# Optimization experiments

Measured on AMD Instinct MI355X. Metric: run time of the kernel, lower is better.

## Reference

```python
import jax, jax.numpy as jnp
import numpy as np

B, S, H, D = 2, 2048, 16, 64
HID = H * D
NEG = -1e9


def _rope(q, cos, sin):
    # q: (B,S,H,D); cos/sin: (S, D//2) -> broadcast (1,S,1,D//2)
    qe, qo = q[..., 0::2], q[..., 1::2]
    c = cos[None, :, None, :]
    s = sin[None, :, None, :]
    oe = qe * c - qo * s
    oo = qe * s + qo * c
    return jnp.stack([oe, oo], axis=-1).reshape(q.shape)  # interleave even/odd pairs


def setup_inputs() -> dict:
    key = jax.random.key(0)
    ks = jax.random.split(key, 9)
    scale = 1.0 / np.sqrt(HID)
    x = jax.random.normal(ks[0], (B, S, HID), jnp.float32)
    Wq = jax.random.normal(ks[1], (HID, HID), jnp.float32) * scale
    Wk = jax.random.normal(ks[2], (HID, HID), jnp.float32) * scale
    Wv = jax.random.normal(ks[3], (HID, HID), jnp.float32) * scale
    Wo = jax.random.normal(ks[4], (HID, HID), jnp.float32) * scale
    bq = jnp.zeros((HID,), jnp.float32)
    bk = jnp.zeros((HID,), jnp.float32)
    bv = jnp.zeros((HID,), jnp.float32)
    bo = jnp.zeros((HID,), jnp.float32)
    # standard RoPE angles: theta_i = 10000^{-2i/D}
    inv_freq = 1.0 / (10000.0 ** (np.arange(0, D, 2, dtype=np.float32) / D))  # (D/2,)
    angles = jnp.arange(S, dtype=jnp.float32)[:, None] * jnp.asarray(inv_freq)[None, :]
    freqs_cos = jnp.cos(angles)
    freqs_sin = jnp.sin(angles)
    causal = jnp.tril(jnp.ones((S, S), bool))
    mask = jnp.where(causal, 0.0, NEG).astype(jnp.float32)[None, None]  # (1,1,S,S)
    return dict(x=x, Wq=Wq, bq=bq, Wk=Wk, bk=bk, Wv=Wv, bv=bv, Wo=Wo, bo=bo,
                mask=mask, freqs_cos=freqs_cos, freqs_sin=freqs_sin)


def reference(x, Wq, bq, Wk, bk, Wv, bv, Wo, bo, mask, freqs_cos, freqs_sin):
    b, s, hid = x.shape
    # weights stored (in, out): y = x @ W + b (equivalent to torch Linear with W^T)
    q = (x @ Wq + bq).reshape(b, s, H, D)
    k = (x @ Wk + bk).reshape(b, s, H, D)
    v = (x @ Wv + bv).reshape(b, s, H, D)
    q = _rope(q, freqs_cos, freqs_sin)
    k = _rope(k, freqs_cos, freqs_sin)
    q = q.transpose(0, 2, 1, 3)  # (B,H,S,D)
    k = k.transpose(0, 2, 1, 3)
    v = v.transpose(0, 2, 1, 3)
    scores = jnp.einsum('bhqd,bhkd->bhqk', q, k) / np.sqrt(D)
    scores = scores + mask
    attn = jax.nn.softmax(scores.astype(jnp.float32), axis=-1)
    out = jnp.einsum('bhqk,bhkd->bhqd', attn, v)
    out = out.transpose(0, 2, 1, 3).reshape(b, s, hid)
    return out @ Wo + bo
```

## Files before the change

### kernel.cpp

```cpp
#include <hip/hip_runtime.h>
#include <hip/hip_bf16.h>

#define BDIM 2
#define SDIM 2048
#define HDIM 16
#define DDIM 64
#define HID  1024
#define MDIM (BDIM * SDIM)

typedef __attribute__((ext_vector_type(8))) short short8;
typedef __attribute__((ext_vector_type(4))) short short4v;
typedef __attribute__((ext_vector_type(4))) float f32x4;
typedef __attribute__((ext_vector_type(2))) unsigned int uint2v;

__device__ __forceinline__ float bf2f(short u) {
    union { unsigned int i; float f; } x;
    x.i = ((unsigned int)(unsigned short)u) << 16;
    return x.f;
}
__device__ __forceinline__ short f2bf(float f) {
    union { float f; unsigned int i; } x; x.f = f;
    unsigned int r = x.i + 0x7fffu + ((x.i >> 16) & 1u);
    return (short)(r >> 16);
}
__device__ __forceinline__ unsigned int cvtpk_bf16(float lo, float hi) {
    unsigned int r;
    asm("v_cvt_pk_bf16_f32 %0, %1, %2" : "=v"(r) : "v"(lo), "v"(hi));
    return r;
}
__device__ __forceinline__ int swz(int row, int c8) {
    return row * 64 + ((c8 ^ (row & 7)) << 3);
}

__global__ __launch_bounds__(256) void cvt_bf16(const float* __restrict__ in,
                                               short* __restrict__ out, int n) {
    int i = (blockIdx.x * 256 + threadIdx.x) * 8;
    if (i >= n) return;
    float4 a = *(const float4*)(in + i);
    float4 b = *(const float4*)(in + i + 4);
    short8 v;
    v[0] = f2bf(a.x); v[1] = f2bf(a.y); v[2] = f2bf(a.z); v[3] = f2bf(a.w);
    v[4] = f2bf(b.x); v[5] = f2bf(b.y); v[6] = f2bf(b.z); v[7] = f2bf(b.w);
    *(short8*)(out + i) = v;
}

__global__ __launch_bounds__(256) void transpose4(
    const float* __restrict__ w0, const float* __restrict__ w1,
    const float* __restrict__ w2, const float* __restrict__ w3,
    short* __restrict__ o0, short* __restrict__ o1,
    short* __restrict__ o2, short* __restrict__ o3)
{
    const float* src; short* dst;
    int z = blockIdx.z;
    if (z == 0)      { src = w0; dst = o0; }
    else if (z == 1) { src = w1; dst = o1; }
    else if (z == 2) { src = w2; dst = o2; }
    else             { src = w3; dst = o3; }
    __shared__ float t[64][65];
    int r0 = blockIdx.y * 64, c0 = blockIdx.x * 64;
    int rd_r = threadIdx.x >> 4, rd_c = (threadIdx.x & 15) * 4;
    #pragma unroll
    for (int it = 0; it < 4; it++) {
        int rr = rd_r + it * 16;
        float4 v = *(const float4*)(src + (size_t)(r0 + rr) * HID + c0 + rd_c);
        t[rr][rd_c + 0] = v.x; t[rr][rd_c + 1] = v.y;
        t[rr][rd_c + 2] = v.z; t[rr][rd_c + 3] = v.w;
    }
    __syncthreads();
    int or_ = threadIdx.x >> 3, oc8 = (threadIdx.x & 7) * 8;
    #pragma unroll
    for (int half = 0; half < 2; half++) {
        int dr = or_ + half * 32;
        short8 v;
        #pragma unroll
        for (int i = 0; i < 8; i++) v[i] = f2bf(t[oc8 + i][dr]);
        *(short8*)(dst + (size_t)(c0 + dr) * HID + r0 + oc8) = v;
    }
}

__global__ __launch_bounds__(256) void gemm_bf16(
    const short* __restrict__ X,
    const short* __restrict__ Wt0,
    const float* __restrict__ b0, const float* __restrict__ b1, const float* __restrict__ b2,
    const float* __restrict__ cosb, const float* __restrict__ sinb,
    short* __restrict__ out0, float* __restrict__ outf,
    int modeBase)
{
    constexpr int LDK = 40;
    __shared__ __align__(16) short Asm[2][128 * LDK];
    __shared__ __align__(16) short Bsm[2][128 * LDK];
    int z = blockIdx.z;
    int mode = modeBase + z;
    const short* Wt = Wt0 + (size_t)z * HID * HID;
    const float* bias = (z == 0) ? b0 : (z == 1) ? b1 : b2;
    short* outp = out0 + (size_t)z * MDIM * HID;

    int tid = threadIdx.x;
    int lane = tid & 63, wave = tid >> 6;
    int wr = wave >> 1, wc = wave & 1;
    int m0 = blockIdx.x * 128, n0 = blockIdx.y * 128;
    int sr = tid >> 2, sc = (tid & 3) * 8;
    int lr = lane & 15, lg = lane >> 4;

    const short* ax = X  + (size_t)(m0 + sr) * HID + sc;
    const short* bx = Wt + (size_t)(n0 + sr) * HID + sc;
    int wA = sr * LDK + sc, wA2 = (sr + 64) * LDK + sc;

    f32x4 acc[4][4] = {};
    constexpr int NK = HID / 32;

    short8 a0, a1, b0v, b1v;
    a0  = *(const short8*)(ax);
    a1  = *(const short8*)(ax + (size_t)64 * HID);
    b0v = *(const short8*)(bx);
    b1v = *(const short8*)(bx + (size_t)64 * HID);
    *(short8*)(Asm[0] + wA)  = a0;
    *(short8*)(Asm[0] + wA2) = a1;
    *(short8*)(Bsm[0] + wA)  = b0v;
    *(short8*)(Bsm[0] + wA2) = b1v;
    a0  = *(const short8*)(ax + 32);
    a1  = *(const short8*)(ax + (size_t)64 * HID + 32);
    b0v = *(const short8*)(bx + 32);
    b1v = *(const short8*)(bx + (size_t)64 * HID + 32);

    int cur = 0;
    for (int ki = 0; ki < NK; ki++) {
        __syncthreads();
        if (ki + 1 < NK) {
            *(short8*)(Asm[cur ^ 1] + wA)  = a0;
            *(short8*)(Asm[cur ^ 1] + wA2) = a1;
            *(short8*)(Bsm[cur ^ 1] + wA)  = b0v;
            *(short8*)(Bsm[cur ^ 1] + wA2) = b1v;
        }
        if (ki + 2 < NK) {
            int k0 = (ki + 2) * 32;
            a0  = *(const short8*)(ax + k0);
            a1  = *(const short8*)(ax + (size_t)64 * HID + k0);
            b0v = *(const short8*)(bx + k0);
            b1v = *(const short8*)(bx + (size_t)64 * HID + k0);
        }
        short8 af[4], bfr[4];
        #pragma unroll
        for (int m = 0; m < 4; m++)
            af[m] = *(const short8*)(Asm[cur] + (wr * 64 + m * 16 + lr) * LDK + lg * 8);
        #pragma unroll
        for (int n = 0; n < 4; n++)
            bfr[n] = *(const short8*)(Bsm[cur] + (wc * 64 + n * 16 + lr) * LDK + lg * 8);
        __builtin_amdgcn_s_setprio(1);
        #pragma unroll
        for (int m = 0; m < 4; m++)
            #pragma unroll
            for (int n = 0; n < 4; n++)
                acc[m][n] = __builtin_amdgcn_mfma_f32_16x16x32_bf16(af[m], bfr[n], acc[m][n], 0, 0, 0);
        __builtin_amdgcn_s_setprio(0);
        cur ^= 1;
    }

    #pragma unroll
    for (int m = 0; m < 4; m++) {
        #pragma unroll
        for (int n = 0; n < 4; n++) {
            int gr0 = m0 + wr * 64 + m * 16 + lg * 4;
            int gc  = n0 + wc * 64 + n * 16 + lr;
            if (mode == 3) {
                #pragma unroll
                for (int j = 0; j < 4; j++)
                    outf[(size_t)(gr0 + j) * HID + gc] = acc[m][n][j] + bias[gc];
            } else if (mode == 2) {
                int bb = gr0 >> 11, s0 = gr0 & (SDIM - 1);
                int h = gc >> 6, dd = gc & 63;
                short4v pk;
                #pragma unroll
                for (int j = 0; j < 4; j++) pk[j] = f2bf(acc[m][n][j] + bias[gc]);
                *(short4v*)(outp + ((size_t)((bb * HDIM + h) * DDIM + dd)) * SDIM + s0) = pk;
            } else {
                #pragma unroll
                for (int j = 0; j < 4; j++) {
                    int gr = gr0 + j;
                    int bb = gr >> 11, s = gr & (SDIM - 1);
                    int h = gc >> 6, dd = gc & 63;
                    float v = acc[m][n][j] + bias[gc];
                    float p  = __shfl_xor(v, 1);
                    float cc = cosb[s * 32 + (dd >> 1)];
                    float ss = sinb[s * 32 + (dd >> 1)];
                    v = (dd & 1) ? (p * ss + v * cc) : (v * cc - p * ss);
                    outp[((size_t)((bb * HDIM + h) * SDIM + s)) * DDIM + dd] = f2bf(v);
                }
            }
        }
    }
}

__global__ __launch_bounds__(512) void attn_fwd(
    const short* __restrict__ Q,
    const short* __restrict__ K,
    const short* __restrict__ Vt,
    short* __restrict__ O)
{
    __shared__ __align__(16) short Ks0[64 * 64], Ks1[64 * 64];
    __shared__ __align__(16) short Vs0[64 * 64], Vs1[64 * 64];
    __shared__ __align__(16) short Ps[8][16 * 64];
    int bx = blockIdx.x;
    int qA = bx, qB = 31 - bx;
    int bh = blockIdx.y;
    int tid = threadIdx.x;
    int lane = tid & 63, wave = tid >> 6;
    int wv = wave & 3, grp = wave >> 2;
    int lr = lane & 15, lg = lane >> 4;
    const short* qbase  = Q  + ((size_t)bh * SDIM) * DDIM;
    const short* kbase  = K  + ((size_t)bh * SDIM) * DDIM;
    const short* vtbase = Vt + ((size_t)bh * DDIM) * SDIM;

    const float SCALE = 0.125f * 1.44269504088896340736f;

    int qt_own = grp ? qA : qB;
    int qrow = qt_own * 64 + wv * 16 + lr;

    short8 qf[2];
    #pragma unroll
    for (int ks = 0; ks < 2; ks++) {
        short8 a = *(const short8*)(qbase + (size_t)qrow * DDIM + ks * 32 + lg * 8);
        short8 ra;
        #pragma unroll
        for (int i = 0; i < 8; i++) ra[i] = f2bf(bf2f(a[i]) * SCALE);
        qf[ks] = ra;
    }

    f32x4 lacc = {0.f, 0.f, 0.f, 0.f};
    f32x4 oacc[4] = {};

    int sr_ = tid >> 3, sc8 = tid & 7;
    int kw = swz(sr_, sc8);
    int fo[8];
    #pragma unroll
    for (int ks = 0; ks < 2; ks++)
        #pragma unroll
        for (int n = 0; n < 4; n++) fo[ks * 4 + n] = swz(n * 16 + lr, ks * 4 + lg);
    int po[2] = { swz(lr, lg), swz(lr, 4 + lg) };
    int pw[4];
    #pragma unroll
    for (int n = 0; n < 4; n++)
        pw[n] = lr * 64 + (((n * 2 + (lg >> 1)) ^ (lr & 7)) << 3) + (lg & 1) * 4;

    int nt = qB + 1;

    short8 kreg, vreg;
    kreg = *(const short8*)(kbase + (size_t)sr_ * DDIM + sc8 * 8);
    vreg = *(const short8*)(vtbase + (size_t)sr_ * SDIM + sc8 * 8);
    *(short8*)(Ks0 + kw) = kreg;
    *(short8*)(Vs0 + kw) = vreg;
    kreg = *(const short8*)(kbase + (size_t)(64 + sr_) * DDIM + sc8 * 8);
    vreg = *(const short8*)(vtbase + (size_t)sr_ * SDIM + 64 + sc8 * 8);
    const short* kpre = kbase + (size_t)(128 + sr_) * DDIM + sc8 * 8;
    const short* vpre = vtbase + (size_t)sr_ * SDIM + 128 + sc8 * 8;

    auto pv = [&](f32x4 (&st)[4], bool diag, int kt, short* VsC) {
        if (diag) {
            #pragma unroll
            for (int n = 0; n < 4; n++)
                #pragma unroll
                for (int j = 0; j < 4; j++) {
                    int k = kt * 64 + n * 16 + lg * 4 + j;
                    if (k > qrow) st[n][j] = -1e30f;
                }
        }
        #pragma unroll
        for (int n = 0; n < 4; n++) {
            #pragma unroll
            for (int j = 0; j < 4; j++) st[n][j] = exp2f(st[n][j]);
            lacc[n] += (st[n][0] + st[n][1]) + (st[n][2] + st[n][3]);
        }
        #pragma unroll
        for (int n = 0; n < 4; n++) {
            uint2v pk;
            pk[0] = cvtpk_bf16(st[n][0], st[n][1]);
            pk[1] = cvtpk_bf16(st[n][2], st[n][3]);
            *(uint2v*)(Ps[wave] + pw[n]) = pk;
        }
        __builtin_amdgcn_s_setprio(1);
        #pragma unroll
        for (int ks = 0; ks < 2; ks++) {
            short8 pf = *(const short8*)(Ps[wave] + po[ks]);
            #pragma unroll
            for (int n = 0; n < 4; n++) {
                short8 vf = *(const short8*)(VsC + fo[ks * 4 + n]);
                oacc[n] = __builtin_amdgcn_mfma_f32_16x16x32_bf16(pf, vf, oacc[n], 0, 0, 0);
            }
        }
        __builtin_amdgcn_s_setprio(0);
    };

    auto tile = [&](int kt, short* KsC, short* VsC, short* KsN, short* VsN) {
        __syncthreads();
        if (kt + 1 < nt) {
            *(short8*)(KsN + kw) = kreg;
            *(short8*)(VsN + kw) = vreg;
        }
        if (kt + 2 < nt) {
            kreg = *(const short8*)(kpre);
            vreg = *(const short8*)(vpre);
        }
        kpre += 64 * DDIM;
        vpre += 64;

        bool act = grp ? (kt <= qA) : true;
        if (act) {
            f32x4 st[4] = {};
            __builtin_amdgcn_s_setprio(1);
            #pragma unroll
            for (int ks = 0; ks < 2; ks++) {
                short8 kf[4];
                #pragma unroll
                for (int n = 0; n < 4; n++) kf[n] = *(const short8*)(KsC + fo[ks * 4 + n]);
                #pragma unroll
                for (int n = 0; n < 4; n++)
                    st[n] = __builtin_amdgcn_mfma_f32_16x16x32_bf16(kf[n], qf[ks], st[n], 0, 0, 0);
            }
            __builtin_amdgcn_s_setprio(0);
            pv(st, kt == qt_own, kt, VsC);
        }
    };

    for (int kt = 0; kt < nt; kt += 2) {
        tile(kt, Ks0, Vs0, Ks1, Vs1);
        if (kt + 1 < nt) tile(kt + 1, Ks1, Vs1, Ks0, Vs0);
    }

    float l = (lacc[0] + lacc[1]) + (lacc[2] + lacc[3]);
    l += __shfl_xor(l, 16);
    l += __shfl_xor(l, 32);
    int b = bh >> 4, h = bh & 15;
    float linv[4];
    #pragma unroll
    for (int j = 0; j < 4; j++)
        linv[j] = 1.f / __int_as_float(__builtin_amdgcn_ds_bpermute((lg * 4 + j) * 4, __float_as_int(l)));
    #pragma unroll
    for (int n = 0; n < 4; n++)
        #pragma unroll
        for (int j = 0; j < 4; j++) {
            int s = qt_own * 64 + wv * 16 + lg * 4 + j;
            int dd = n * 16 + lr;
            O[(((size_t)(b * SDIM + s) * HDIM) + h) * DDIM + dd] = f2bf(oacc[n][j] * linv[j]);
        }
}

extern "C" void kernel_launch(void* const* d_in, const int* in_sizes, int n_in,
                              void* d_out, int out_size, void* d_ws, size_t ws_size,
                              hipStream_t stream) {
    const float* x  = (const float*)d_in[0];
    const float* Wq = (const float*)d_in[1];
    const float* bq = (const float*)d_in[2];
    const float* Wk = (const float*)d_in[3];
    const float* bk = (const float*)d_in[4];
    const float* Wv = (const float*)d_in[5];
    const float* bv = (const float*)d_in[6];
    const float* Wo = (const float*)d_in[7];
    const float* bo = (const float*)d_in[8];
    const float* fc = (const float*)d_in[10];
    const float* fs = (const float*)d_in[11];
    float* out = (float*)d_out;
    short* ws  = (short*)d_ws;

    const size_t MM = (size_t)HID * HID;
    short* xb     = ws;
    short* wt_qkv = ws + 4 * MM;
    short* wot    = ws + 7 * MM;
    short* qt     = ws + 8 * MM;
    short* ktb    = ws + 12 * MM;
    short* vtb    = ws + 16 * MM;
    short* ao     = ws + 20 * MM;

    cvt_bf16<<<dim3((MDIM * HID) / (256 * 8)), 256, 0, stream>>>(x, xb, MDIM * HID);
    transpose4<<<dim3(16, 16, 4), 256, 0, stream>>>(Wq, Wk, Wv, Wo,
                                                    wt_qkv, wt_qkv + MM, wt_qkv + 2 * MM, wot);
    gemm_bf16<<<dim3(MDIM / 128, HID / 128, 3), 256, 0, stream>>>(
        xb, wt_qkv, bq, bk, bv, fc, fs, qt, nullptr, 0);
    attn_fwd<<<dim3(16, BDIM * HDIM), 512, 0, stream>>>(qt, ktb, vtb, ao);
    gemm_bf16<<<dim3(MDIM / 128, HID / 128, 1), 256, 0, stream>>>(
        ao, wot, bo, bo, bo, fc, fs, nullptr, out, 3);
}
```

Baseline: 111.0 us.

## Load GEMM tiles directly into LDS with global_load_lds and XOR swizzle

Replaces the register-staged global-to-shared copy in the bf16 GEMM with direct global_load_lds transfers into LDS. The padded layout is swapped for an unpadded 32-wide layout with an XOR column swizzle on both the write and read sides. This saves VGPRs and the separate LDS store instructions, and it moves the barrier to the end of each iteration. In exchange, prefetch depth drops from two stages ahead to one, which could expose more global latency.

Result: slower. 136.8 us (+23.3%).

```diff
diff --git a/kernel.cpp b/kernel.cpp
--- a/kernel.cpp
+++ b/kernel.cpp
@@ -27,6 +27,11 @@
     unsigned int r;
     asm("v_cvt_pk_bf16_f32 %0, %1, %2" : "=v"(r) : "v"(lo), "v"(hi));
     return r;
+}
+__device__ __forceinline__ void glds16(const short* g, short* l) {
+    __builtin_amdgcn_global_load_lds(
+        (const __attribute__((address_space(1))) unsigned int*)g,
+        (__attribute__((address_space(3))) unsigned int*)l, 16, 0, 0);
 }
 __device__ __forceinline__ int swz(int row, int c8) {
     return row * 64 + ((c8 ^ (row & 7)) << 3);
@@ -86,9 +91,8 @@
     short* __restrict__ out0, float* __restrict__ outf,
     int modeBase)
 {
-    constexpr int LDK = 40;
-    __shared__ __align__(16) short Asm[2][128 * LDK];
-    __shared__ __align__(16) short Bsm[2][128 * LDK];
+    __shared__ __align__(16) short Asm[2][128 * 32];
+    __shared__ __align__(16) short Bsm[2][128 * 32];
     int z = blockIdx.z;
     int mode = modeBase + z;
     const short* Wt = Wt0 + (size_t)z * HID * HID;
@@ -99,53 +103,43 @@
     int lane = tid & 63, wave = tid >> 6;
     int wr = wave >> 1, wc = wave & 1;
     int m0 = blockIdx.x * 128, n0 = blockIdx.y * 128;
-    int sr = tid >> 2, sc = (tid & 3) * 8;
     int lr = lane & 15, lg = lane >> 4;
 
-    const short* ax = X  + (size_t)(m0 + sr) * HID + sc;
-    const short* bx = Wt + (size_t)(n0 + sr) * HID + sc;
-    int wA = sr * LDK + sc, wA2 = (sr + 64) * LDK + sc;
+    int lrow = lane >> 2;
+    int csw  = (lane & 3) ^ (lrow & 3);
+    const short* ag0 = X  + (size_t)(m0 + wave * 32 + lrow) * HID + csw * 8;
+    const short* ag1 = ag0 + (size_t)16 * HID;
+    const short* bg0 = Wt + (size_t)(n0 + wave * 32 + lrow) * HID + csw * 8;
+    const short* bg1 = bg0 + (size_t)16 * HID;
+    int woff = wave * 1024;
+
+    int rdsw = (lg ^ (lr & 3)) * 8;
 
     f32x4 acc[4][4] = {};
     constexpr int NK = HID / 32;
 
-    short8 a0, a1, b0v, b1v;
-    a0  = *(const short8*)(ax);
-    a1  = *(const short8*)(ax + (size_t)64 * HID);
-    b0v = *(const short8*)(bx);
-    b1v = *(const short8*)(bx + (size_t)64 * HID);
-    *(short8*)(Asm[0] + wA)  = a0;
-    *(short8*)(Asm[0] + wA2) = a1;
-    *(short8*)(Bsm[0] + wA)  = b0v;
-    *(short8*)(Bsm[0] + wA2) = b1v;
-    a0  = *(const short8*)(ax + 32);
-    a1  = *(const short8*)(ax + (size_t)64 * HID + 32);
-    b0v = *(const short8*)(bx + 32);
-    b1v = *(const short8*)(bx + (size_t)64 * HID + 32);
+    glds16(ag0, Asm[0] + woff);
+    glds16(ag1, Asm[0] + woff + 512);
+    glds16(bg0, Bsm[0] + woff);
+    glds16(bg1, Bsm[0] + woff + 512);
+    __syncthreads();
 
     int cur = 0;
     for (int ki = 0; ki < NK; ki++) {
-        __syncthreads();
         if (ki + 1 < NK) {
-            *(short8*)(Asm[cur ^ 1] + wA)  = a0;
-            *(short8*)(Asm[cur ^ 1] + wA2) = a1;
-            *(short8*)(Bsm[cur ^ 1] + wA)  = b0v;
-            *(short8*)(Bsm[cur ^ 1] + wA2) = b1v;
-        }
-        if (ki + 2 < NK) {
-            int k0 = (ki + 2) * 32;
-            a0  = *(const short8*)(ax + k0);
-            a1  = *(const short8*)(ax + (size_t)64 * HID + k0);
-            b0v = *(const short8*)(bx + k0);
-            b1v = *(const short8*)(bx + (size_t)64 * HID + k0);
+            int k0 = (ki + 1) * 32;
+            glds16(ag0 + k0, Asm[cur ^ 1] + woff);
+            glds16(ag1 + k0, Asm[cur ^ 1] + woff + 512);
+            glds16(bg0 + k0, Bsm[cur ^ 1] + woff);
+            glds16(bg1 + k0, Bsm[cur ^ 1] + woff + 512);
         }
         short8 af[4], bfr[4];
         #pragma unroll
         for (int m = 0; m < 4; m++)
-            af[m] = *(const short8*)(Asm[cur] + (wr * 64 + m * 16 + lr) * LDK + lg * 8);
+            af[m] = *(const short8*)(Asm[cur] + (wr * 64 + m * 16 + lr) * 32 + rdsw);
         #pragma unroll
         for (int n = 0; n < 4; n++)
-            bfr[n] = *(const short8*)(Bsm[cur] + (wc * 64 + n * 16 + lr) * LDK + lg * 8);
+            bfr[n] = *(const short8*)(Bsm[cur] + (wc * 64 + n * 16 + lr) * 32 + rdsw);
         __builtin_amdgcn_s_setprio(1);
         #pragma unroll
         for (int m = 0; m < 4; m++)
@@ -153,6 +147,7 @@
             for (int n = 0; n < 4; n++)
                 acc[m][n] = __builtin_amdgcn_mfma_f32_16x16x32_bf16(af[m], bfr[n], acc[m][n], 0, 0, 0);
         __builtin_amdgcn_s_setprio(0);
+        __syncthreads();
         cur ^= 1;
     }
 
```

## Fuse fp32-to-bf16 input conversion into QKV GEMM and swizzle block order

Applied to the files above, without the earlier changes.

Removes the standalone cvt_bf16 kernel. The QKV GEMM now loads fp32 activations directly and converts them to bf16 in registers before writing to shared memory, which saves a kernel launch and a round trip of the bf16 copy through global memory. In exchange, each QKV block reads twice the activation bytes, and all three z-slices redo the conversion. It also remaps block indices so groups of 8 consecutive blocks share tiles, aiming for better L2 reuse.

New measurement: 126.5 us. +14.0%, slower.

```diff
diff --git a/kernel.cpp b/kernel.cpp
--- a/kernel.cpp
+++ b/kernel.cpp
@@ -1,5 +1,6 @@
 #include <hip/hip_runtime.h>
 #include <hip/hip_bf16.h>
+#include <type_traits>
 
 #define BDIM 2
 #define SDIM 2048
@@ -11,6 +12,7 @@
 typedef __attribute__((ext_vector_type(8))) short short8;
 typedef __attribute__((ext_vector_type(4))) short short4v;
 typedef __attribute__((ext_vector_type(4))) float f32x4;
+typedef __attribute__((ext_vector_type(8))) float f32x8;
 typedef __attribute__((ext_vector_type(2))) unsigned int uint2v;
 
 __device__ __forceinline__ float bf2f(short u) {
@@ -28,20 +30,15 @@
     asm("v_cvt_pk_bf16_f32 %0, %1, %2" : "=v"(r) : "v"(lo), "v"(hi));
     return r;
 }
+__device__ __forceinline__ short8 toBf8(short8 v) { return v; }
+__device__ __forceinline__ short8 toBf8(f32x8 v) {
+    short8 s;
+    #pragma unroll
+    for (int i = 0; i < 8; i++) s[i] = f2bf(v[i]);
+    return s;
+}
 __device__ __forceinline__ int swz(int row, int c8) {
     return row * 64 + ((c8 ^ (row & 7)) << 3);
-}
-
-__global__ __launch_bounds__(256) void cvt_bf16(const float* __restrict__ in,
-                                               short* __restrict__ out, int n) {
-    int i = (blockIdx.x * 256 + threadIdx.x) * 8;
-    if (i >= n) return;
-    float4 a = *(const float4*)(in + i);
-    float4 b = *(const float4*)(in + i + 4);
-    short8 v;
-    v[0] = f2bf(a.x); v[1] = f2bf(a.y); v[2] = f2bf(a.z); v[3] = f2bf(a.w);
-    v[4] = f2bf(b.x); v[5] = f2bf(b.y); v[6] = f2bf(b.z); v[7] = f2bf(b.w);
-    *(short8*)(out + i) = v;
 }
 
 __global__ __launch_bounds__(256) void transpose4(
@@ -78,48 +75,57 @@
     }
 }
 
+template<bool AF32>
 __global__ __launch_bounds__(256) void gemm_bf16(
-    const short* __restrict__ X,
+    const void* __restrict__ Xv,
     const short* __restrict__ Wt0,
     const float* __restrict__ b0, const float* __restrict__ b1, const float* __restrict__ b2,
     const float* __restrict__ cosb, const float* __restrict__ sinb,
     short* __restrict__ out0, float* __restrict__ outf,
     int modeBase)
 {
+    using aelem_t = std::conditional_t<AF32, float, short>;
+    using areg_t  = std::conditional_t<AF32, f32x8, short8>;
     constexpr int LDK = 40;
     __shared__ __align__(16) short Asm[2][128 * LDK];
     __shared__ __align__(16) short Bsm[2][128 * LDK];
     int z = blockIdx.z;
     int mode = modeBase + z;
+    const aelem_t* X = (const aelem_t*)Xv;
     const short* Wt = Wt0 + (size_t)z * HID * HID;
     const float* bias = (z == 0) ? b0 : (z == 1) ? b1 : b2;
     short* outp = out0 + (size_t)z * MDIM * HID;
 
+    int idx = blockIdx.y * gridDim.x + blockIdx.x;
+    int sw  = (idx & 7) * 32 + (idx >> 3);
+    int m_blk = sw & 31, n_blk = sw >> 5;
+
     int tid = threadIdx.x;
     int lane = tid & 63, wave = tid >> 6;
     int wr = wave >> 1, wc = wave & 1;
-    int m0 = blockIdx.x * 128, n0 = blockIdx.y * 128;
+    int m0 = m_blk * 128, n0 = n_blk * 128;
     int sr = tid >> 2, sc = (tid & 3) * 8;
     int lr = lane & 15, lg = lane >> 4;
 
-    const short* ax = X  + (size_t)(m0 + sr) * HID + sc;
-    const short* bx = Wt + (size_t)(n0 + sr) * HID + sc;
+    const aelem_t* ax = X  + (size_t)(m0 + sr) * HID + sc;
+    const short*   bx = Wt + (size_t)(n0 + sr) * HID + sc;
     int wA = sr * LDK + sc, wA2 = (sr + 64) * LDK + sc;
 
     f32x4 acc[4][4] = {};
     constexpr int NK = HID / 32;
 
-    short8 a0, a1, b0v, b1v;
-    a0  = *(const short8*)(ax);
-    a1  = *(const short8*)(ax + (size_t)64 * HID);
+    areg_t a0, a1;
+    short8 b0v, b1v;
+    a0  = *(const areg_t*)(ax);
+    a1  = *(const areg_t*)(ax + (size_t)64 * HID);
     b0v = *(const short8*)(bx);
     b1v = *(const short8*)(bx + (size_t)64 * HID);
-    *(short8*)(Asm[0] + wA)  = a0;
-    *(short8*)(Asm[0] + wA2) = a1;
+    *(short8*)(Asm[0] + wA)  = toBf8(a0);
+    *(short8*)(Asm[0] + wA2) = toBf8(a1);
     *(short8*)(Bsm[0] + wA)  = b0v;
     *(short8*)(Bsm[0] + wA2) = b1v;
-    a0  = *(const short8*)(ax + 32);
-    a1  = *(const short8*)(ax + (size_t)64 * HID + 32);
+    a0  = *(const areg_t*)(ax + 32);
+    a1  = *(const areg_t*)(ax + (size_t)64 * HID + 32);
     b0v = *(const short8*)(bx + 32);
     b1v = *(const short8*)(bx + (size_t)64 * HID + 32);
 
@@ -127,15 +133,15 @@
     for (int ki = 0; ki < NK; ki++) {
         __syncthreads();
         if (ki + 1 < NK) {
-            *(short8*)(Asm[cur ^ 1] + wA)  = a0;
-            *(short8*)(Asm[cur ^ 1] + wA2) = a1;
+            *(short8*)(Asm[cur ^ 1] + wA)  = toBf8(a0);
+            *(short8*)(Asm[cur ^ 1] + wA2) = toBf8(a1);
             *(short8*)(Bsm[cur ^ 1] + wA)  = b0v;
             *(short8*)(Bsm[cur ^ 1] + wA2) = b1v;
         }
         if (ki + 2 < NK) {
             int k0 = (ki + 2) * 32;
-            a0  = *(const short8*)(ax + k0);
-            a1  = *(const short8*)(ax + (size_t)64 * HID + k0);
+            a0  = *(const areg_t*)(ax + k0);
+            a1  = *(const areg_t*)(ax + (size_t)64 * HID + k0);
             b0v = *(const short8*)(bx + k0);
             b1v = *(const short8*)(bx + (size_t)64 * HID + k0);
         }
@@ -362,7 +368,6 @@
     short* ws  = (short*)d_ws;
 
     const size_t MM = (size_t)HID * HID;
-    short* xb     = ws;
     short* wt_qkv = ws + 4 * MM;
     short* wot    = ws + 7 * MM;
     short* qt     = ws + 8 * MM;
@@ -370,12 +375,11 @@
     short* vtb    = ws + 16 * MM;
     short* ao     = ws + 20 * MM;
 
-    cvt_bf16<<<dim3((MDIM * HID) / (256 * 8)), 256, 0, stream>>>(x, xb, MDIM * HID);
     transpose4<<<dim3(16, 16, 4), 256, 0, stream>>>(Wq, Wk, Wv, Wo,
                                                     wt_qkv, wt_qkv + MM, wt_qkv + 2 * MM, wot);
-    gemm_bf16<<<dim3(MDIM / 128, HID / 128, 3), 256, 0, stream>>>(
-        xb, wt_qkv, bq, bk, bv, fc, fs, qt, nullptr, 0);
+    gemm_bf16<true><<<dim3(MDIM / 128, HID / 128, 3), 256, 0, stream>>>(
+        x, wt_qkv, bq, bk, bv, fc, fs, qt, nullptr, 0);
     attn_fwd<<<dim3(16, BDIM * HDIM), 512, 0, stream>>>(qt, ktb, vtb, ao);
-    gemm_bf16<<<dim3(MDIM / 128, HID / 128, 1), 256, 0, stream>>>(
+    gemm_bf16<false><<<dim3(MDIM / 128, HID / 128, 1), 256, 0, stream>>>(
         ao, wot, bo, bo, bo, fc, fs, nullptr, out, 3);
 }
```
